# Kernel tuning notes

Hardware: AMD Instinct MI355X
Metric: run time of the kernel (lower is better)

Reference implementation:

```python
import jax, jax.numpy as jnp
import numpy as np

NUM_VARS = 22
LAYERS = 2
N = 2 ** NUM_VARS


def setup_inputs() -> dict:
    key = jax.random.key(0)
    k1, k2, k3, k4 = jax.random.split(key, 4)
    h = jax.random.normal(k1, (N,), dtype=jnp.float32)          # unsatisfied-clause 'energy' per bitstring
    hS = jax.random.uniform(k2, (N,), dtype=jnp.float32)        # satisfiability weight per bitstring
    gamma = jax.random.normal(k3, (LAYERS,), dtype=jnp.float32) * 0.01
    beta = jax.random.normal(k4, (LAYERS,), dtype=jnp.float32) * 0.01
    return {"h": h, "hS": hS, "gamma": gamma, "beta": beta}


def reference(h, hS, gamma, beta):
    n = NUM_VARS
    # |+>^n initial state: uniform amplitudes 1/sqrt(N)
    circuit = jnp.full((N,), 1.0 / np.sqrt(N), dtype=jnp.complex64)
    for l in range(LAYERS):
        # cost unitary: elementwise phase exp(i * gamma * h)
        circuit = jnp.exp((1j * gamma[l] * h).astype(jnp.complex64)) * circuit
        # mixing unitary: per-qubit X-rotation butterfly.
        # torch's transpose(0,i)+split+cat swaps the two slices along qubit axis i,
        # which for a size-2 axis is exactly a flip along that axis.
        cb = jnp.cos(beta[l]).astype(jnp.complex64)
        sb = (1j * jnp.sin(beta[l])).astype(jnp.complex64)
        c = circuit.reshape((2,) * n)
        for i in range(n):  # fixed small loop over qubits (structurally distinct axes)
            c = cb * c + sb * jnp.flip(c, axis=i)
        circuit = c.reshape(N)
    ps = jnp.real(circuit * jnp.conj(circuit))  # |amplitude|^2
    return jnp.dot(ps, hS)
```

## Files before the change

kernel.cpp:

```cpp
#include <hip/hip_runtime.h>


#define NTOT    (1u << 22)
#define LO_BITS 13
#define HI_BITS 9
#define LO      (1u << LO_BITS)
#define HI      (1u << HI_BITS)
#define GRP     16
#define TPB     512
#define R       16

typedef __fp16 h2_t __attribute__((ext_vector_type(2)));
union PkU { unsigned u; h2_t h; };

__device__ __forceinline__ unsigned pk(float x, float y) {
    PkU p; p.h = __builtin_amdgcn_cvt_pkrtz(x, y); return p.u;
}
__device__ __forceinline__ float2 unpk(unsigned v) {
    PkU p; p.u = v; return make_float2((float)p.h.x, (float)p.h.y);
}

#define REGSTAGE(MASK, CB, SB) {                                  \
    _Pragma("unroll")                                             \
    for (int r0 = 0; r0 < R; ++r0) {                              \
        if ((r0 & (MASK)) == 0) {                                 \
            const int r1 = r0 | (MASK);                           \
            float t0r = re[r0], t0i = im[r0];                     \
            float t1r = re[r1], t1i = im[r1];                     \
            re[r0] = (CB) * t0r - (SB) * t1i;                     \
            im[r0] = (CB) * t0i + (SB) * t1r;                     \
            re[r1] = (CB) * t1r - (SB) * t0i;                     \
            im[r1] = (CB) * t1i + (SB) * t0r;                     \
        } } }

#define SHFLSTAGE(MASK, CB, SB) {                                 \
    _Pragma("unroll")                                             \
    for (int r = 0; r < R; ++r) {                                 \
        unsigned pv = (unsigned)__shfl_xor((int)pk(re[r], im[r]), (MASK), 64); \
        float2 p = unpk(pv);                                      \
        float tr = re[r], ti = im[r];                             \
        re[r] = (CB) * tr - (SB) * p.y;                           \
        im[r] = (CB) * ti + (SB) * p.x;                           \
    } }

__global__ __launch_bounds__(TPB, 4) void k_init_low(
    const float* __restrict__ h, const float* __restrict__ gam,
    const float* __restrict__ bet, unsigned* __restrict__ st,
    float* __restrict__ out)
{
    __shared__ unsigned sC[LO];
    const float g1 = gam[0];
    const float cb = __cosf(bet[0]), sb = __sinf(bet[0]);
    const unsigned t = threadIdx.x, lane = t & 63u, wave = t >> 6;
    const size_t base = (size_t)blockIdx.x * LO;
    float re[R], im[R];

    if (blockIdx.x == 0 && t == 0) out[0] = 0.f;

    #pragma unroll
    for (int r = 0; r < R; ++r) {
        float s, c;
        __sincosf(g1 * h[base + (unsigned)r * TPB + t], &s, &c);
        re[r] = c * 0x1p-11f;
        im[r] = s * 0x1p-11f;
    }
    REGSTAGE(1, cb, sb)  REGSTAGE(2, cb, sb)
    REGSTAGE(4, cb, sb)  REGSTAGE(8, cb, sb)
    SHFLSTAGE(1,  cb, sb) SHFLSTAGE(2,  cb, sb)
    SHFLSTAGE(4,  cb, sb) SHFLSTAGE(8,  cb, sb)
    SHFLSTAGE(16, cb, sb) SHFLSTAGE(32, cb, sb)
    #pragma unroll
    for (int r = 0; r < R; ++r) sC[(unsigned)r * TPB + t] = pk(re[r], im[r]);
    __syncthreads();
    #pragma unroll
    for (int r = 0; r < R; ++r) {
        unsigned j = lane | ((unsigned)(r & 7) << 6) | (wave << 9) | ((unsigned)(r >> 3) << 12);
        float2 v = unpk(sC[j]); re[r] = v.x; im[r] = v.y;
    }
    REGSTAGE(1, cb, sb)  REGSTAGE(2, cb, sb)  REGSTAGE(4, cb, sb)
    #pragma unroll
    for (int r = 0; r < R; ++r) {
        unsigned j = lane | ((unsigned)(r & 7) << 6) | (wave << 9) | ((unsigned)(r >> 3) << 12);
        st[base + j] = pk(re[r], im[r]);
    }
}

__global__ __launch_bounds__(TPB, 4) void k_high(
    const float* __restrict__ h, const float* __restrict__ gam,
    const float* __restrict__ bet, unsigned* __restrict__ st)
{
    __shared__ unsigned sC[GRP * HI];
    const float g2  = gam[1];
    const float cb1 = __cosf(bet[0]), sb1 = __sinf(bet[0]);
    const float cb2 = __cosf(bet[1]), sb2 = __sinf(bet[1]);
    const unsigned t = threadIdx.x, lane = t & 63u, wave = t >> 6;
    const unsigned lo0 = blockIdx.x * GRP;
    const unsigned g   = lane & (GRP - 1);
    const unsigned h01 = lane >> 4;
    float re[R], im[R];

    #pragma unroll
    for (int r = 0; r < R; ++r) {
        unsigned hi = h01 | (wave << 2) | ((unsigned)r << 5);
        float2 v = unpk(st[(size_t)hi * LO + lo0 + g]);
        re[r] = v.x; im[r] = v.y;
    }
    REGSTAGE(1, cb1, sb1)  REGSTAGE(2, cb1, sb1)
    REGSTAGE(4, cb1, sb1)  REGSTAGE(8, cb1, sb1)
    SHFLSTAGE(16, cb1, sb1) SHFLSTAGE(32, cb1, sb1)
    #pragma unroll
    for (int r = 0; r < R; ++r) {
        unsigned li = g | (h01 << 4) | (wave << 6) | ((unsigned)r << 9);
        sC[li] = pk(re[r], im[r]);
    }
    __syncthreads();
    #pragma unroll
    for (int r = 0; r < R; ++r) {
        unsigned li = g | (h01 << 4) | ((unsigned)(r & 7) << 6) | (wave << 9) | ((unsigned)(r >> 3) << 12);
        float2 v = unpk(sC[li]); re[r] = v.x; im[r] = v.y;
    }
    REGSTAGE(1, cb1, sb1)  REGSTAGE(2, cb1, sb1)  REGSTAGE(4, cb1, sb1)
    #pragma unroll
    for (int r = 0; r < R; ++r) {
        unsigned hi = h01 | ((unsigned)(r & 7) << 2) | (wave << 5) | ((unsigned)(r >> 3) << 8);
        float s, c;
        __sincosf(g2 * h[(size_t)hi * LO + lo0 + g], &s, &c);
        float tr = re[r], ti = im[r];
        re[r] = tr * c - ti * s;
        im[r] = tr * s + ti * c;
    }
    REGSTAGE(1, cb2, sb2)  REGSTAGE(2, cb2, sb2)
    REGSTAGE(4, cb2, sb2)  REGSTAGE(8, cb2, sb2)
    SHFLSTAGE(16, cb2, sb2) SHFLSTAGE(32, cb2, sb2)
    __syncthreads();
    #pragma unroll
    for (int r = 0; r < R; ++r) {
        unsigned li = g | (h01 << 4) | ((unsigned)(r & 7) << 6) | (wave << 9) | ((unsigned)(r >> 3) << 12);
        sC[li] = pk(re[r], im[r]);
    }
    __syncthreads();
    #pragma unroll
    for (int r = 0; r < R; ++r) {
        unsigned li = g | (h01 << 4) | (wave << 6) | ((unsigned)r << 9);
        float2 v = unpk(sC[li]); re[r] = v.x; im[r] = v.y;
    }
    REGSTAGE(1, cb2, sb2)  REGSTAGE(2, cb2, sb2)  REGSTAGE(4, cb2, sb2)
    #pragma unroll
    for (int r = 0; r < R; ++r) {
        unsigned hi = h01 | (wave << 2) | ((unsigned)r << 5);
        st[(size_t)hi * LO + lo0 + g] = pk(re[r], im[r]);
    }
}

__global__ __launch_bounds__(TPB, 4) void k_low2(
    const float* __restrict__ hS, const float* __restrict__ bet,
    const unsigned* __restrict__ st, float* __restrict__ out)
{
    __shared__ unsigned sC[LO];
    __shared__ float wsum[TPB / 64];
    const float cb = __cosf(bet[1]), sb = __sinf(bet[1]);
    const unsigned t = threadIdx.x, lane = t & 63u, wave = t >> 6;
    const size_t base = (size_t)blockIdx.x * LO;
    float re[R], im[R];

    #pragma unroll
    for (int r = 0; r < R; ++r) {
        float2 v = unpk(st[base + (unsigned)r * TPB + t]);
        re[r] = v.x; im[r] = v.y;
    }
    REGSTAGE(1, cb, sb)  REGSTAGE(2, cb, sb)
    REGSTAGE(4, cb, sb)  REGSTAGE(8, cb, sb)
    SHFLSTAGE(1,  cb, sb) SHFLSTAGE(2,  cb, sb)
    SHFLSTAGE(4,  cb, sb) SHFLSTAGE(8,  cb, sb)
    SHFLSTAGE(16, cb, sb) SHFLSTAGE(32, cb, sb)
    #pragma unroll
    for (int r = 0; r < R; ++r) sC[(unsigned)r * TPB + t] = pk(re[r], im[r]);
    __syncthreads();
    #pragma unroll
    for (int r = 0; r < R; ++r) {
        unsigned j = lane | ((unsigned)(r & 7) << 6) | (wave << 9) | ((unsigned)(r >> 3) << 12);
        float2 v = unpk(sC[j]); re[r] = v.x; im[r] = v.y;
    }
    REGSTAGE(1, cb, sb)  REGSTAGE(2, cb, sb)  REGSTAGE(4, cb, sb)
    float acc = 0.f;
    #pragma unroll
    for (int r = 0; r < R; ++r) {
        unsigned j = lane | ((unsigned)(r & 7) << 6) | (wave << 9) | ((unsigned)(r >> 3) << 12);
        acc = fmaf(re[r] * re[r] + im[r] * im[r], hS[base + j], acc);
    }
    #pragma unroll
    for (int off = 32; off >= 1; off >>= 1)
        acc += __shfl_down(acc, off, 64);
    if (lane == 0) wsum[wave] = acc;
    __syncthreads();
    if (t == 0) {
        float s = 0.f;
        #pragma unroll
        for (int w = 0; w < TPB / 64; ++w) s += wsum[w];
        unsafeAtomicAdd(out, s);
    }
}

extern "C" void kernel_launch(void* const* d_in, const int* in_sizes, int n_in,
                              void* d_out, int out_size, void* d_ws, size_t ws_size,
                              hipStream_t stream)
{
    (void)in_sizes; (void)n_in; (void)out_size; (void)ws_size;
    const float* h   = (const float*)d_in[0];
    const float* hS  = (const float*)d_in[1];
    const float* gam = (const float*)d_in[2];
    const float* bet = (const float*)d_in[3];
    unsigned* st = (unsigned*)d_ws;
    float* out   = (float*)d_out;

    k_init_low<<<dim3(NTOT / LO), dim3(TPB), 0, stream>>>(h, gam, bet, st, out);
    k_high    <<<dim3(LO / GRP),  dim3(TPB), 0, stream>>>(h, gam, bet, st);
    k_low2    <<<dim3(NTOT / LO), dim3(TPB), 0, stream>>>(hS, bet, st, out);
}
```

Measured before the change: 125.9 us.

## Widen k_high column group to 32 and use 1024-thread blocks

k_high now handles 32 low-index columns per block with 1024 threads. Each wave covers two high-bit rows of 32 contiguous columns, so global loads and stores become 128-byte contiguous segments instead of 64-byte ones. The high-bit butterfly is regrouped as 4 register stages, 1 shuffle stage, an LDS transpose, then 4 more register stages, replacing the old 4+2 shuffles plus 3-stage split. This cuts the number of shuffle stages and improves coalescing, at the cost of larger blocks and a doubled shared buffer (64 KB). Launch bounds of 1024 threads with min 4 blocks may cap registers and fewer blocks are launched.

```diff
diff --git a/kernel.cpp b/kernel.cpp
--- a/kernel.cpp
+++ b/kernel.cpp
@@ -6,8 +6,9 @@
 #define HI_BITS 9
 #define LO      (1u << LO_BITS)
 #define HI      (1u << HI_BITS)
-#define GRP     16
+#define GRP     32
 #define TPB     512
+#define TPB2    1024
 #define R       16
 
 typedef __fp16 h2_t __attribute__((ext_vector_type(2)));
@@ -85,7 +86,7 @@
     }
 }
 
-__global__ __launch_bounds__(TPB, 4) void k_high(
+__global__ __launch_bounds__(TPB2, 4) void k_high(
     const float* __restrict__ h, const float* __restrict__ gam,
     const float* __restrict__ bet, unsigned* __restrict__ st)
 {
@@ -93,36 +94,35 @@
     const float g2  = gam[1];
     const float cb1 = __cosf(bet[0]), sb1 = __sinf(bet[0]);
     const float cb2 = __cosf(bet[1]), sb2 = __sinf(bet[1]);
-    const unsigned t = threadIdx.x, lane = t & 63u, wave = t >> 6;
+    const unsigned t = threadIdx.x, lane = t & 63u, w = t >> 6;
+    const unsigned g  = lane & 31u;
+    const unsigned h0 = lane >> 5;
     const unsigned lo0 = blockIdx.x * GRP;
-    const unsigned g   = lane & (GRP - 1);
-    const unsigned h01 = lane >> 4;
     float re[R], im[R];
 
     #pragma unroll
     for (int r = 0; r < R; ++r) {
-        unsigned hi = h01 | (wave << 2) | ((unsigned)r << 5);
+        unsigned hi = h0 | (w << 1) | ((unsigned)r << 5);
         float2 v = unpk(st[(size_t)hi * LO + lo0 + g]);
         re[r] = v.x; im[r] = v.y;
     }
     REGSTAGE(1, cb1, sb1)  REGSTAGE(2, cb1, sb1)
     REGSTAGE(4, cb1, sb1)  REGSTAGE(8, cb1, sb1)
-    SHFLSTAGE(16, cb1, sb1) SHFLSTAGE(32, cb1, sb1)
-    #pragma unroll
-    for (int r = 0; r < R; ++r) {
-        unsigned li = g | (h01 << 4) | (wave << 6) | ((unsigned)r << 9);
-        sC[li] = pk(re[r], im[r]);
-    }
-    __syncthreads();
-    #pragma unroll
-    for (int r = 0; r < R; ++r) {
-        unsigned li = g | (h01 << 4) | ((unsigned)(r & 7) << 6) | (wave << 9) | ((unsigned)(r >> 3) << 12);
-        float2 v = unpk(sC[li]); re[r] = v.x; im[r] = v.y;
-    }
-    REGSTAGE(1, cb1, sb1)  REGSTAGE(2, cb1, sb1)  REGSTAGE(4, cb1, sb1)
-    #pragma unroll
-    for (int r = 0; r < R; ++r) {
-        unsigned hi = h01 | ((unsigned)(r & 7) << 2) | (wave << 5) | ((unsigned)(r >> 3) << 8);
+    SHFLSTAGE(32, cb1, sb1)
+    #pragma unroll
+    for (int r = 0; r < R; ++r)
+        sC[g | (h0 << 5) | (w << 6) | ((unsigned)r << 10)] = pk(re[r], im[r]);
+    __syncthreads();
+    #pragma unroll
+    for (int r = 0; r < R; ++r) {
+        float2 v = unpk(sC[g | (h0 << 5) | ((unsigned)r << 6) | (w << 10)]);
+        re[r] = v.x; im[r] = v.y;
+    }
+    REGSTAGE(1, cb1, sb1)  REGSTAGE(2, cb1, sb1)
+    REGSTAGE(4, cb1, sb1)  REGSTAGE(8, cb1, sb1)
+    #pragma unroll
+    for (int r = 0; r < R; ++r) {
+        unsigned hi = h0 | ((unsigned)r << 1) | (w << 5);
         float s, c;
         __sincosf(g2 * h[(size_t)hi * LO + lo0 + g], &s, &c);
         float tr = re[r], ti = im[r];
@@ -131,23 +131,22 @@
     }
     REGSTAGE(1, cb2, sb2)  REGSTAGE(2, cb2, sb2)
     REGSTAGE(4, cb2, sb2)  REGSTAGE(8, cb2, sb2)
-    SHFLSTAGE(16, cb2, sb2) SHFLSTAGE(32, cb2, sb2)
-    __syncthreads();
-    #pragma unroll
-    for (int r = 0; r < R; ++r) {
-        unsigned li = g | (h01 << 4) | ((unsigned)(r & 7) << 6) | (wave << 9) | ((unsigned)(r >> 3) << 12);
-        sC[li] = pk(re[r], im[r]);
-    }
-    __syncthreads();
-    #pragma unroll
-    for (int r = 0; r < R; ++r) {
-        unsigned li = g | (h01 << 4) | (wave << 6) | ((unsigned)r << 9);
-        float2 v = unpk(sC[li]); re[r] = v.x; im[r] = v.y;
-    }
-    REGSTAGE(1, cb2, sb2)  REGSTAGE(2, cb2, sb2)  REGSTAGE(4, cb2, sb2)
-    #pragma unroll
-    for (int r = 0; r < R; ++r) {
-        unsigned hi = h01 | (wave << 2) | ((unsigned)r << 5);
+    SHFLSTAGE(32, cb2, sb2)
+    __syncthreads();
+    #pragma unroll
+    for (int r = 0; r < R; ++r)
+        sC[g | (h0 << 5) | ((unsigned)r << 6) | (w << 10)] = pk(re[r], im[r]);
+    __syncthreads();
+    #pragma unroll
+    for (int r = 0; r < R; ++r) {
+        float2 v = unpk(sC[g | (h0 << 5) | (w << 6) | ((unsigned)r << 10)]);
+        re[r] = v.x; im[r] = v.y;
+    }
+    REGSTAGE(1, cb2, sb2)  REGSTAGE(2, cb2, sb2)
+    REGSTAGE(4, cb2, sb2)  REGSTAGE(8, cb2, sb2)
+    #pragma unroll
+    for (int r = 0; r < R; ++r) {
+        unsigned hi = h0 | (w << 1) | ((unsigned)r << 5);
         st[(size_t)hi * LO + lo0 + g] = pk(re[r], im[r]);
     }
 }
@@ -213,7 +212,7 @@
     unsigned* st = (unsigned*)d_ws;
     float* out   = (float*)d_out;
 
-    k_init_low<<<dim3(NTOT / LO), dim3(TPB), 0, stream>>>(h, gam, bet, st, out);
-    k_high    <<<dim3(LO / GRP),  dim3(TPB), 0, stream>>>(h, gam, bet, st);
-    k_low2    <<<dim3(NTOT / LO), dim3(TPB), 0, stream>>>(hS, bet, st, out);
-}
+    k_init_low<<<dim3(NTOT / LO), dim3(TPB),  0, stream>>>(h, gam, bet, st, out);
+    k_high    <<<dim3(LO / GRP),  dim3(TPB2), 0, stream>>>(h, gam, bet, st);
+    k_low2    <<<dim3(NTOT / LO), dim3(TPB),  0, stream>>>(hS, bet, st, out);
+}
```

After: 120.9 us. 4.0% less time.
